# Kernel tuning notes

Measured on AMD Instinct MI355X. Metric: run time of the kernel, lower is better.

The kernel has to match this reference:

```python
import jax, jax.numpy as jnp
import numpy as np

S, D, H, F = 4096, 2048, 16, 8192
HD = D // H
EPS = 1e-5


def setup_inputs() -> dict:
    key = jax.random.key(0)
    ks = jax.random.split(key, 16)
    sc_d = 1.0 / np.sqrt(D)
    sc_f = 1.0 / np.sqrt(F)
    return {
        "x": jax.random.normal(ks[0], (S, D), dtype=jnp.float32),
        # stacked per-head projections: [H, D, HD]
        "Wq": jax.random.normal(ks[1], (H, D, HD), dtype=jnp.float32) * sc_d,
        "bq": jax.random.normal(ks[2], (H, HD), dtype=jnp.float32) * 0.01,
        "Wk": jax.random.normal(ks[3], (H, D, HD), dtype=jnp.float32) * sc_d,
        "bk": jax.random.normal(ks[4], (H, HD), dtype=jnp.float32) * 0.01,
        "Wv": jax.random.normal(ks[5], (H, D, HD), dtype=jnp.float32) * sc_d,
        "bv": jax.random.normal(ks[6], (H, HD), dtype=jnp.float32) * 0.01,
        "Wp": jax.random.normal(ks[7], (D, D), dtype=jnp.float32) * sc_d,
        "bp": jax.random.normal(ks[8], (D,), dtype=jnp.float32) * 0.01,
        "W1": jax.random.normal(ks[9], (D, F), dtype=jnp.float32) * sc_d,
        "b1": jax.random.normal(ks[10], (F,), dtype=jnp.float32) * 0.01,
        "W2": jax.random.normal(ks[11], (F, D), dtype=jnp.float32) * sc_f,
        "b2": jax.random.normal(ks[12], (D,), dtype=jnp.float32) * 0.01,
        "gamma": jnp.ones((D,), dtype=jnp.float32),
        "beta": jnp.zeros((D,), dtype=jnp.float32),
    }


def _layernorm(x, gamma, beta):
    mu = jnp.mean(x, axis=-1, keepdims=True)
    var = jnp.var(x, axis=-1, keepdims=True)
    return (x - mu) * jax.lax.rsqrt(var + EPS) * gamma + beta


def reference(x, Wq, bq, Wk, bk, Wv, bv, Wp, bp, W1, b1, W2, b2, gamma, beta):
    residual = x
    # batched per-head projections: [H, S, HD]
    q = jnp.einsum('sd,hde->hse', x, Wq) + bq[:, None, :]
    k = jnp.einsum('sd,hde->hse', x, Wk) + bk[:, None, :]
    v = jnp.einsum('sd,hde->hse', x, Wv) + bv[:, None, :]
    scores = jnp.einsum('hse,hte->hst', q, k) / np.sqrt(HD).astype(np.float32)
    attn = jax.nn.softmax(scores, axis=-1)
    heads = jnp.einsum('hst,hte->hse', attn, v)  # [H, S, HD]
    # concat heads along feature dim (head 0 first): [S, H*HD]
    heads = jnp.transpose(heads, (1, 0, 2)).reshape(S, H * HD)
    out = heads @ Wp + bp
    # residual_attn=True, norm_attn=True
    out = out + residual
    out = _layernorm(out, gamma, beta)
    # feedforward (original forward ends here)
    out = jax.nn.relu(out @ W1 + b1) @ W2 + b2
    return out
```

## Files before the change

### kernel.cpp

```cpp
#include <hip/hip_runtime.h>
#include <hip/hip_bf16.h>
#include <cstdint>
#include <cstddef>

#define S 4096
#define D 2048
#define H 16
#define HD 128
#define F 8192

typedef unsigned short ushort_t;
typedef __attribute__((ext_vector_type(8))) short short8;
typedef __attribute__((ext_vector_type(4))) float floatx4;

__device__ __forceinline__ ushort_t f2bf(float f) {
  union { float f; unsigned u; } v; v.f = f;
  unsigned u = v.u;
  return (ushort_t)((u + 0x7fffu + ((u >> 16) & 1u)) >> 16);
}

__device__ __forceinline__ void async16(void* lds, const void* g) {
  __builtin_amdgcn_global_load_lds(
      (const __attribute__((address_space(1))) unsigned int*)g,
      (__attribute__((address_space(3))) unsigned int*)lds, 16, 0, 0);
}

template <int N>
__device__ __forceinline__ void vmcnt_() {
  static_assert(N >= 0 && N <= 8, "vmcnt range");
  if constexpr (N == 0) asm volatile("s_waitcnt vmcnt(0)" ::: "memory");
  else if constexpr (N == 1) asm volatile("s_waitcnt vmcnt(1)" ::: "memory");
  else if constexpr (N == 2) asm volatile("s_waitcnt vmcnt(2)" ::: "memory");
  else if constexpr (N == 3) asm volatile("s_waitcnt vmcnt(3)" ::: "memory");
  else if constexpr (N == 4) asm volatile("s_waitcnt vmcnt(4)" ::: "memory");
  else if constexpr (N == 5) asm volatile("s_waitcnt vmcnt(5)" ::: "memory");
  else if constexpr (N == 6) asm volatile("s_waitcnt vmcnt(6)" ::: "memory");
  else if constexpr (N == 7) asm volatile("s_waitcnt vmcnt(7)" ::: "memory");
  else asm volatile("s_waitcnt vmcnt(8)" ::: "memory");
}
__device__ __forceinline__ void bar_() { asm volatile("s_barrier" ::: "memory"); }
__device__ __forceinline__ void lgkm0_() {
  asm volatile("s_waitcnt lgkmcnt(0)" ::: "memory");
  __builtin_amdgcn_sched_barrier(0);
}


__global__ void cast_bf16(const float* __restrict__ src, ushort_t* __restrict__ dst, int n4) {
  int i = blockIdx.x * blockDim.x + threadIdx.x;
  if (i < n4) {
    float4 v = ((const float4*)src)[i];
    ushort4 o;
    o.x = f2bf(v.x); o.y = f2bf(v.y); o.z = f2bf(v.z); o.w = f2bf(v.w);
    ((ushort4*)dst)[i] = o;
  }
}

__global__ void build_bqkv(const float* __restrict__ bq, const float* __restrict__ bk,
                           const float* __restrict__ bv, float* __restrict__ bqkv) {
  int n = blockIdx.x * blockDim.x + threadIdx.x;
  if (n < 3 * D) {
    float v;
    if (n < D) v = bq[n];
    else if (n < 2 * D) v = bk[n - D];
    else v = bv[n - 2 * D];
    bqkv[n] = v;
  }
}

__global__ void transpose_f32_bf16(const float* __restrict__ src, ushort_t* __restrict__ dst,
                                   int ldS, int ldD, long srcBatchStride, long dstBatchRows) {
  __shared__ float t[32][33];
  int b = blockIdx.z;
  src += (size_t)b * srcBatchStride;
  dst += (size_t)b * dstBatchRows * ldD;
  int r0 = blockIdx.x * 32, c0 = blockIdx.y * 32;
  int tx = threadIdx.x, ty = threadIdx.y;
#pragma unroll
  for (int i = 0; i < 4; ++i)
    t[ty + i * 8][tx] = src[(size_t)(r0 + ty + i * 8) * ldS + c0 + tx];
  __syncthreads();
#pragma unroll
  for (int i = 0; i < 4; ++i)
    dst[(size_t)(c0 + ty + i * 8) * ldD + r0 + tx] = f2bf(t[tx][ty + i * 8]);
}

__global__ void transpose_bf16(const ushort_t* __restrict__ src, ushort_t* __restrict__ dst,
                               int ldS, int ldD, int colOff) {
  __shared__ ushort_t t[32][33];
  int r0 = blockIdx.x * 32, c0 = blockIdx.y * 32;
  int tx = threadIdx.x, ty = threadIdx.y;
#pragma unroll
  for (int i = 0; i < 4; ++i)
    t[ty + i * 8][tx] = src[(size_t)(r0 + ty + i * 8) * ldS + colOff + c0 + tx];
  __syncthreads();
#pragma unroll
  for (int i = 0; i < 4; ++i)
    dst[(size_t)(c0 + ty + i * 8) * ldD + r0 + tx] = t[tx][ty + i * 8];
}

template <int MODE, int BM>
__global__ __launch_bounds__(512, 2)
void gemm8p(const ushort_t* __restrict__ A, const ushort_t* __restrict__ Bt,
            const float* __restrict__ bias, const float* __restrict__ resid,
            ushort_t* __restrict__ outb, float* __restrict__ outf,
            int M, int N, int K, int gridN) {
  constexpr int MQ = BM / 64;
  constexpr int LA = BM / 128;
  __shared__ __align__(16) ushort_t Abuf[2][BM * 64];
  __shared__ __align__(16) ushort_t Bbuf[2][256 * 64];

  const int tid = threadIdx.x;
  const int l = tid & 63, w = tid >> 6;
  const int c16 = l & 15, g = l >> 4;
  const int wm = w >> 2, wn = w & 3;

  const int nwg = gridDim.x;
  const int q8 = nwg >> 3, r8 = nwg & 7;
  const int xcd = blockIdx.x & 7, bix = blockIdx.x >> 3;
  const int wgid = (xcd < r8 ? xcd * (q8 + 1) : r8 * (q8 + 1) + (xcd - r8) * q8) + bix;
  const int m0 = (wgid / gridN) * BM;
  const int n0 = (wgid % gridN) * 256;

  const size_t Kb = (size_t)K * 2;
  const size_t aHalfB = (size_t)(BM / 2) * Kb;
  const size_t bHalfB = (size_t)128 * Kb;

  const char* aSrc[LA]; char* aLds[LA];
#pragma unroll
  for (int i = 0; i < LA; ++i) {
    int ch = i * 512 + tid;
    int row = ch >> 3;
    aSrc[i] = (const char*)A + (size_t)(m0 + row) * Kb + (((ch ^ row) & 7) << 4);
    aLds[i] = (char*)(&Abuf[0][0]) + ch * 16;
  }
  const char* bSrc[2]; char* bLds[2];
#pragma unroll
  for (int i = 0; i < 2; ++i) {
    int ch = i * 512 + tid;
    int row = ch >> 3;
    bSrc[i] = (const char*)Bt + (size_t)(n0 + row) * Kb + (((ch ^ row) & 7) << 4);
    bLds[i] = (char*)(&Bbuf[0][0]) + ch * 16;
  }

  auto stA = [&](int p, int h, int kByte) {
#pragma unroll
    for (int i = 0; i < LA; ++i)
      async16(aLds[i] + p * (BM * 128) + h * (BM * 64), aSrc[i] + (size_t)h * aHalfB + kByte);
  };
  auto stB = [&](int p, int h, int kByte) {
#pragma unroll
    for (int i = 0; i < 2; ++i)
      async16(bLds[i] + p * 32768 + h * 16384, bSrc[i] + (size_t)h * bHalfB + kByte);
  };

  int rdK[2];
  rdK[0] = ((g ^ (c16 & 7)) << 4);
  rdK[1] = (((4 + g) ^ (c16 & 7)) << 4);
  const char* Ab0 = (const char*)(&Abuf[0][0]);
  const char* Ab1 = Ab0 + BM * 128;
  const char* Bb0 = (const char*)(&Bbuf[0][0]);
  const char* Bb1 = Bb0 + 32768;

  floatx4 acc[2][2][MQ][2];
#pragma unroll
  for (int ah = 0; ah < 2; ++ah)
#pragma unroll
    for (int bh = 0; bh < 2; ++bh)
#pragma unroll
      for (int mf = 0; mf < MQ; ++mf)
#pragma unroll
        for (int nf = 0; nf < 2; ++nf) acc[ah][bh][mf][nf] = (floatx4){0.f, 0.f, 0.f, 0.f};

  short8 af[MQ][2], bf0[2][2], bf1[2][2];
  auto ldA = [&](const char* base, int h) {
#pragma unroll
    for (int mf = 0; mf < MQ; ++mf)
#pragma unroll
      for (int kk = 0; kk < 2; ++kk)
        af[mf][kk] = *(const short8*)(base + h * (BM * 64) +
            (wm * (BM / 4) + mf * 16 + c16) * 128 + rdK[kk]);
  };
  auto ldB = [&](const char* base, int h, short8 (&bf)[2][2]) {
#pragma unroll
    for (int nf = 0; nf < 2; ++nf)
#pragma unroll
      for (int kk = 0; kk < 2; ++kk)
        bf[nf][kk] = *(const short8*)(base + h * 16384 +
            (wn * 32 + nf * 16 + c16) * 128 + rdK[kk]);
  };
  auto mma2 = [&](int ah) {
    __builtin_amdgcn_s_setprio(1);
#pragma unroll
    for (int mf = 0; mf < MQ; ++mf)
#pragma unroll
      for (int kk = 0; kk < 2; ++kk) {
#pragma unroll
        for (int nf = 0; nf < 2; ++nf)
          acc[ah][0][mf][nf] = __builtin_amdgcn_mfma_f32_16x16x32_bf16(
              af[mf][kk], bf0[nf][kk], acc[ah][0][mf][nf], 0, 0, 0);
#pragma unroll
        for (int nf = 0; nf < 2; ++nf)
          acc[ah][1][mf][nf] = __builtin_amdgcn_mfma_f32_16x16x32_bf16(
              af[mf][kk], bf1[nf][kk], acc[ah][1][mf][nf], 0, 0, 0);
      }
    __builtin_amdgcn_s_setprio(0);
  };

  stA(0, 0, 0); stB(0, 0, 0); stB(0, 1, 0); stA(0, 1, 0);
  stA(1, 0, 128); stB(1, 0, 128); stB(1, 1, 128);
  vmcnt_<LA + 4>();
  bar_();

  const int NI = K >> 7;
  for (int i = 0; i < NI; ++i) {
    const bool lastI = (i == NI - 1);
    const int kE = i << 8;

    ldA(Ab0, 0); ldB(Bb0, 0, bf0); ldB(Bb0, 1, bf1);
    stA(1, 1, kE + 128);
    bar_(); lgkm0_();
    mma2(0);
    bar_();

    ldA(Ab0, 1);
    if (!lastI) { stA(0, 0, kE + 256); stB(0, 0, kE + 256); stB(0, 1, kE + 256); }
    bar_(); lgkm0_();
    mma2(1);
    if (lastI) vmcnt_<0>(); else vmcnt_<LA + 4>();
    bar_();

    ldA(Ab1, 0); ldB(Bb1, 0, bf0); ldB(Bb1, 1, bf1);
    if (!lastI) stA(0, 1, kE + 256);
    bar_(); lgkm0_();
    mma2(0);
    bar_();

    ldA(Ab1, 1);
    if (!lastI) { stA(1, 0, kE + 384); stB(1, 0, kE + 384); stB(1, 1, kE + 384); }
    bar_(); lgkm0_();
    mma2(1);
    if (!lastI) { vmcnt_<LA + 4>(); bar_(); }
  }

#pragma unroll
  for (int ah = 0; ah < 2; ++ah)
#pragma unroll
    for (int bh = 0; bh < 2; ++bh)
#pragma unroll
      for (int nf = 0; nf < 2; ++nf) {
        int gcol = n0 + bh * 128 + wn * 32 + nf * 16 + c16;
        float bj = bias[gcol];
#pragma unroll
        for (int mf = 0; mf < MQ; ++mf) {
          int grow = m0 + ah * (BM / 2) + wm * (BM / 4) + mf * 16 + g * 4;
#pragma unroll
          for (int r = 0; r < 4; ++r) {
            float v = acc[ah][bh][mf][nf][r] + bj;
            size_t o = (size_t)(grow + r) * N + gcol;
            if (MODE == 0) {
              outb[o] = f2bf(v);
            } else if (MODE == 1) {
              outf[o] = v + resid[o];
            } else if (MODE == 2) {
              outb[o] = f2bf(v > 0.f ? v : 0.f);
            } else {
              outf[o] = v;
            }
          }
        }
      }
}

__global__ __launch_bounds__(256, 2)
void attn_kernel(const ushort_t* __restrict__ QKV, const ushort_t* __restrict__ Vt,
                 ushort_t* __restrict__ heads) {
  const int h = blockIdx.y;
  const int tid = threadIdx.x, w = tid >> 6, l = tid & 63;
  const int g = l >> 4, c = l & 15;
  const int q0 = blockIdx.x * 128 + w * 32;
  const float scale = 0.08838834764831845f;

  __shared__ __align__(16) ushort_t Ks[64 * 128];
  __shared__ __align__(16) ushort_t Vs[128 * 64];
  __shared__ __align__(16) ushort_t Ps[4][2][16][72];

  short8 qf[2][4];
#pragma unroll
  for (int u = 0; u < 2; ++u)
#pragma unroll
    for (int k0 = 0; k0 < 4; ++k0)
      qf[u][k0] = *(const short8*)(QKV + (size_t)(q0 + u * 16 + c) * (3 * D) + h * HD + k0 * 32 + g * 8);

  floatx4 o[2][8];
#pragma unroll
  for (int u = 0; u < 2; ++u)
#pragma unroll
    for (int j = 0; j < 8; ++j) o[u][j] = (floatx4){0.f, 0.f, 0.f, 0.f};
  float l_run[2] = {0.f, 0.f};

  for (int t0 = 0; t0 < S; t0 += 64) {
#pragma unroll
    for (int cc = 0; cc < 4; ++cc) {
      int slot = cc * 256 + tid;
      int krow = slot >> 4, kch = slot & 15;
      const char* gk = (const char*)QKV +
          ((size_t)(t0 + krow) * (3 * D) + D + h * HD) * 2 + ((kch ^ (krow & 15)) << 4);
      async16((char*)Ks + (size_t)(cc * 256 + w * 64) * 16, gk);
      int vrow = slot >> 3, vch = slot & 7;
      const char* gv = (const char*)Vt +
          ((size_t)(h * HD + vrow) * S + t0) * 2 + ((vch ^ (vrow & 7)) << 4);
      async16((char*)Vs + (size_t)(cc * 256 + w * 64) * 16, gv);
    }
    __syncthreads();

    floatx4 sc[2][4];
#pragma unroll
    for (int u = 0; u < 2; ++u)
#pragma unroll
      for (int tt = 0; tt < 4; ++tt) sc[u][tt] = (floatx4){0.f, 0.f, 0.f, 0.f};
#pragma unroll
    for (int tt = 0; tt < 4; ++tt) {
      short8 kf[4];
#pragma unroll
      for (int k0 = 0; k0 < 4; ++k0)
        kf[k0] = *(const short8*)(Ks + (tt * 16 + c) * 128 + (((k0 * 4 + g) ^ c) << 3));
#pragma unroll
      for (int u = 0; u < 2; ++u)
#pragma unroll
        for (int k0 = 0; k0 < 4; ++k0)
          sc[u][tt] = __builtin_amdgcn_mfma_f32_16x16x32_bf16(kf[k0], qf[u][k0], sc[u][tt], 0, 0, 0);
    }

#pragma unroll
    for (int u = 0; u < 2; ++u) {
#pragma unroll
      for (int tt = 0; tt < 4; ++tt) {
        float p0 = __expf(sc[u][tt][0] * scale);
        float p1 = __expf(sc[u][tt][1] * scale);
        float p2 = __expf(sc[u][tt][2] * scale);
        float p3 = __expf(sc[u][tt][3] * scale);
        l_run[u] += p0 + p1 + p2 + p3;
        ushort4 pk;
        pk.x = f2bf(p0); pk.y = f2bf(p1); pk.z = f2bf(p2); pk.w = f2bf(p3);
        *reinterpret_cast<ushort4*>(&Ps[w][u][c][tt * 16 + g * 4]) = pk;
      }
    }
    __asm__ volatile("s_waitcnt lgkmcnt(0)" ::: "memory");

    short8 pf[2][2];
#pragma unroll
    for (int u = 0; u < 2; ++u)
#pragma unroll
      for (int tk = 0; tk < 2; ++tk)
        pf[u][tk] = *reinterpret_cast<const short8*>(&Ps[w][u][c][tk * 32 + g * 8]);
#pragma unroll
    for (int j = 0; j < 8; ++j) {
#pragma unroll
      for (int tk = 0; tk < 2; ++tk) {
        short8 vf = *(const short8*)(Vs + (j * 16 + c) * 64 + (((tk * 4 + g) ^ (c & 7)) << 3));
#pragma unroll
        for (int u = 0; u < 2; ++u)
          o[u][j] = __builtin_amdgcn_mfma_f32_16x16x32_bf16(pf[u][tk], vf, o[u][j], 0, 0, 0);
      }
    }
    __syncthreads();
  }

#pragma unroll
  for (int u = 0; u < 2; ++u) {
    float lt = l_run[u];
    lt += __shfl_xor(lt, 16);
    lt += __shfl_xor(lt, 32);
    float linv[4];
#pragma unroll
    for (int r = 0; r < 4; ++r) linv[r] = 1.f / __shfl(lt, g * 4 + r);
    ushort_t* hp = heads + (size_t)(q0 + u * 16 + g * 4) * D + h * HD + c;
#pragma unroll
    for (int j = 0; j < 8; ++j)
#pragma unroll
      for (int r = 0; r < 4; ++r)
        hp[(size_t)r * D + j * 16] = f2bf(o[u][j][r] * linv[r]);
  }
}

__global__ __launch_bounds__(256)
void ln_kernel(const float* __restrict__ preln, const float* __restrict__ gamma,
               const float* __restrict__ beta, ushort_t* __restrict__ y) {
  int row = blockIdx.x, tid = threadIdx.x;
  const float* p = preln + (size_t)row * D;
  float vals[8];
  float sum = 0.f, ss = 0.f;
#pragma unroll
  for (int k = 0; k < 8; ++k) {
    float v = p[tid + k * 256];
    vals[k] = v; sum += v; ss += v * v;
  }
#pragma unroll
  for (int off = 32; off >= 1; off >>= 1) {
    sum += __shfl_xor(sum, off);
    ss += __shfl_xor(ss, off);
  }
  __shared__ float s1[4], s2[4];
  int w = tid >> 6, l = tid & 63;
  if (l == 0) { s1[w] = sum; s2[w] = ss; }
  __syncthreads();
  sum = s1[0] + s1[1] + s1[2] + s1[3];
  ss = s2[0] + s2[1] + s2[2] + s2[3];
  float mu = sum / (float)D;
  float var = ss / (float)D - mu * mu;
  float rs = rsqrtf(var + 1e-5f);
  ushort_t* yr = y + (size_t)row * D;
#pragma unroll
  for (int k = 0; k < 8; ++k) {
    int d = tid + k * 256;
    yr[d] = f2bf((vals[k] - mu) * rs * gamma[d] + beta[d]);
  }
}


extern "C" void kernel_launch(void* const* d_in, const int* in_sizes, int n_in,
                              void* d_out, int out_size, void* d_ws, size_t ws_size,
                              hipStream_t stream) {
  const float* x = (const float*)d_in[0];
  const float* Wq = (const float*)d_in[1];
  const float* bq = (const float*)d_in[2];
  const float* Wk = (const float*)d_in[3];
  const float* bk = (const float*)d_in[4];
  const float* Wv = (const float*)d_in[5];
  const float* bv = (const float*)d_in[6];
  const float* Wp = (const float*)d_in[7];
  const float* bp = (const float*)d_in[8];
  const float* W1 = (const float*)d_in[9];
  const float* b1 = (const float*)d_in[10];
  const float* W2 = (const float*)d_in[11];
  const float* b2 = (const float*)d_in[12];
  const float* gamma = (const float*)d_in[13];
  const float* beta = (const float*)d_in[14];

  char* ws = (char*)d_ws;
  ushort_t* WQKVT = (ushort_t*)(ws + 0);
  ushort_t* XB    = (ushort_t*)(ws + 25165824);
  float*    BQKV  = (float*)(ws + 41943040);
  ushort_t* WPT   = (ushort_t*)(ws + 41975808);
  ushort_t* W1T   = (ushort_t*)(ws + 50364416);
  ushort_t* W2T   = (ushort_t*)(ws + 83918848);
  ushort_t* QKV   = (ushort_t*)(ws + 117473280);
  ushort_t* HEADS = (ushort_t*)(ws + 167804928);
  ushort_t* VT    = (ushort_t*)(ws + 184582144);
  float*    PRELN = (float*)(ws + 0);
  ushort_t* AB    = (ushort_t*)(ws + 117473280);
  ushort_t* Y     = (ushort_t*)(ws + 184582144);
  float* OUT = (float*)d_out;

  dim3 tb(32, 8);
  cast_bf16<<<(S * D / 4 + 255) / 256, 256, 0, stream>>>(x, XB, S * D / 4);
  build_bqkv<<<(3 * D + 255) / 256, 256, 0, stream>>>(bq, bk, bv, BQKV);
  transpose_f32_bf16<<<dim3(D / 32, HD / 32, H), tb, 0, stream>>>(Wq, WQKVT, HD, D, (long)D * HD, HD);
  transpose_f32_bf16<<<dim3(D / 32, HD / 32, H), tb, 0, stream>>>(Wk, WQKVT + (size_t)D * D, HD, D, (long)D * HD, HD);
  transpose_f32_bf16<<<dim3(D / 32, HD / 32, H), tb, 0, stream>>>(Wv, WQKVT + (size_t)2 * D * D, HD, D, (long)D * HD, HD);
  transpose_f32_bf16<<<dim3(D / 32, D / 32, 1), tb, 0, stream>>>(Wp, WPT, D, D, 0, 0);
  transpose_f32_bf16<<<dim3(D / 32, F / 32, 1), tb, 0, stream>>>(W1, W1T, F, D, 0, 0);
  transpose_f32_bf16<<<dim3(F / 32, D / 32, 1), tb, 0, stream>>>(W2, W2T, D, F, 0, 0);
  gemm8p<0, 256><<<dim3((S / 256) * (3 * D / 256)), 512, 0, stream>>>(
      XB, WQKVT, BQKV, nullptr, QKV, nullptr, S, 3 * D, D, 3 * D / 256);
  transpose_bf16<<<dim3(S / 32, D / 32), tb, 0, stream>>>(QKV, VT, 3 * D, S, 2 * D);
  attn_kernel<<<dim3(S / 128, H), 256, 0, stream>>>(QKV, VT, HEADS);
  gemm8p<1, 128><<<dim3((S / 128) * (D / 256)), 512, 0, stream>>>(
      HEADS, WPT, bp, x, nullptr, PRELN, S, D, D, D / 256);
  ln_kernel<<<S, 256, 0, stream>>>(PRELN, gamma, beta, Y);
  gemm8p<2, 256><<<dim3((S / 256) * (F / 256)), 512, 0, stream>>>(
      Y, W1T, b1, nullptr, AB, nullptr, S, F, D, F / 256);
  gemm8p<3, 128><<<dim3((S / 128) * (D / 256)), 512, 0, stream>>>(
      AB, W2T, b2, nullptr, nullptr, OUT, S, D, F, D / 256);
}
```

Baseline: 915.0 us.

## Double-buffer K tiles in attention and overlap V loads with QK compute

The attention kernel now double-buffers the K tile in shared memory, prefetching the next K block while the current one is used. V loads are issued at the start of each iteration and waited on only after the QK^T and softmax stage, using explicit vmcnt waits and barriers instead of __syncthreads. The aim is to hide global-to-LDS load latency behind the MFMA work, at the cost of more LDS, which may lower occupancy. The bf16 packing of P now uses v_cvt_pk_bf16_f32, and the QKV GEMM tile size changes from 256 to 128 rows.

```diff
diff --git a/kernel.cpp b/kernel.cpp
--- a/kernel.cpp
+++ b/kernel.cpp
@@ -280,7 +280,7 @@
   const int q0 = blockIdx.x * 128 + w * 32;
   const float scale = 0.08838834764831845f;
 
-  __shared__ __align__(16) ushort_t Ks[64 * 128];
+  __shared__ __align__(16) ushort_t Ks[2][64 * 128];
   __shared__ __align__(16) ushort_t Vs[128 * 64];
   __shared__ __align__(16) ushort_t Ps[4][2][16][72];
 
@@ -298,21 +298,41 @@
     for (int j = 0; j < 8; ++j) o[u][j] = (floatx4){0.f, 0.f, 0.f, 0.f};
   float l_run[2] = {0.f, 0.f};
 
-  for (int t0 = 0; t0 < S; t0 += 64) {
+#pragma unroll
+  for (int cc = 0; cc < 4; ++cc) {
+    int slot = cc * 256 + tid;
+    int krow = slot >> 4, kch = slot & 15;
+    const char* gk = (const char*)QKV +
+        ((size_t)krow * (3 * D) + D + h * HD) * 2 + ((kch ^ (krow & 15)) << 4);
+    async16((char*)(&Ks[0][0]) + (size_t)(cc * 256 + w * 64) * 16, gk);
+  }
+
+  for (int t0 = 0, ti = 0; t0 < S; t0 += 64, ++ti) {
+    const int cur = ti & 1, nxt = cur ^ 1;
+    const bool lastT = (t0 + 64 >= S);
+
 #pragma unroll
     for (int cc = 0; cc < 4; ++cc) {
       int slot = cc * 256 + tid;
-      int krow = slot >> 4, kch = slot & 15;
-      const char* gk = (const char*)QKV +
-          ((size_t)(t0 + krow) * (3 * D) + D + h * HD) * 2 + ((kch ^ (krow & 15)) << 4);
-      async16((char*)Ks + (size_t)(cc * 256 + w * 64) * 16, gk);
       int vrow = slot >> 3, vch = slot & 7;
       const char* gv = (const char*)Vt +
           ((size_t)(h * HD + vrow) * S + t0) * 2 + ((vch ^ (vrow & 7)) << 4);
       async16((char*)Vs + (size_t)(cc * 256 + w * 64) * 16, gv);
     }
-    __syncthreads();
-
+    if (!lastT) {
+#pragma unroll
+      for (int cc = 0; cc < 4; ++cc) {
+        int slot = cc * 256 + tid;
+        int krow = slot >> 4, kch = slot & 15;
+        const char* gk = (const char*)QKV +
+            ((size_t)(t0 + 64 + krow) * (3 * D) + D + h * HD) * 2 + ((kch ^ (krow & 15)) << 4);
+        async16((char*)(&Ks[0][0]) + (size_t)(nxt * 1024 + cc * 256 + w * 64) * 16, gk);
+      }
+    }
+    if (lastT) vmcnt_<4>(); else vmcnt_<8>();
+    bar_();
+
+    const ushort_t* Kb = &Ks[cur][0];
     floatx4 sc[2][4];
 #pragma unroll
     for (int u = 0; u < 2; ++u)
@@ -323,7 +343,7 @@
       short8 kf[4];
 #pragma unroll
       for (int k0 = 0; k0 < 4; ++k0)
-        kf[k0] = *(const short8*)(Ks + (tt * 16 + c) * 128 + (((k0 * 4 + g) ^ c) << 3));
+        kf[k0] = *(const short8*)(Kb + (tt * 16 + c) * 128 + (((k0 * 4 + g) ^ c) << 3));
 #pragma unroll
       for (int u = 0; u < 2; ++u)
 #pragma unroll
@@ -340,12 +360,16 @@
         float p2 = __expf(sc[u][tt][2] * scale);
         float p3 = __expf(sc[u][tt][3] * scale);
         l_run[u] += p0 + p1 + p2 + p3;
-        ushort4 pk;
-        pk.x = f2bf(p0); pk.y = f2bf(p1); pk.z = f2bf(p2); pk.w = f2bf(p3);
-        *reinterpret_cast<ushort4*>(&Ps[w][u][c][tt * 16 + g * 4]) = pk;
+        unsigned r0, r1;
+        asm("v_cvt_pk_bf16_f32 %0, %1, %2" : "=v"(r0) : "v"(p0), "v"(p1));
+        asm("v_cvt_pk_bf16_f32 %0, %1, %2" : "=v"(r1) : "v"(p2), "v"(p3));
+        uint2 pk; pk.x = r0; pk.y = r1;
+        *reinterpret_cast<uint2*>(&Ps[w][u][c][tt * 16 + g * 4]) = pk;
       }
     }
     __asm__ volatile("s_waitcnt lgkmcnt(0)" ::: "memory");
+    if (lastT) vmcnt_<0>(); else vmcnt_<4>();
+    bar_();
 
     short8 pf[2][2];
 #pragma unroll
@@ -363,7 +387,7 @@
           o[u][j] = __builtin_amdgcn_mfma_f32_16x16x32_bf16(pf[u][tk], vf, o[u][j], 0, 0, 0);
       }
     }
-    __syncthreads();
+    bar_();
   }
 
 #pragma unroll
@@ -461,7 +485,7 @@
   transpose_f32_bf16<<<dim3(D / 32, D / 32, 1), tb, 0, stream>>>(Wp, WPT, D, D, 0, 0);
   transpose_f32_bf16<<<dim3(D / 32, F / 32, 1), tb, 0, stream>>>(W1, W1T, F, D, 0, 0);
   transpose_f32_bf16<<<dim3(F / 32, D / 32, 1), tb, 0, stream>>>(W2, W2T, D, F, 0, 0);
-  gemm8p<0, 256><<<dim3((S / 256) * (3 * D / 256)), 512, 0, stream>>>(
+  gemm8p<0, 128><<<dim3((S / 128) * (3 * D / 256)), 512, 0, stream>>>(
       XB, WQKVT, BQKV, nullptr, QKV, nullptr, S, 3 * D, D, 3 * D / 256);
   transpose_bf16<<<dim3(S / 32, D / 32), tb, 0, stream>>>(QKV, VT, 3 * D, S, 2 * D);
   attn_kernel<<<dim3(S / 128, H), 256, 0, stream>>>(QKV, VT, HEADS);
```

After: 926.8 us. Within noise of the previous version (+1.3%).
